# Kernel optimization log

Measured on AMD Instinct MI355X. Metric: run time of the kernel, lower is better.

Reference implementation:

```python
import jax, jax.numpy as jnp
import numpy as np

B, C, D, H, W = 2, 128, 16, 16, 16
DSIM = PSIM = GDIM = 64
N_ROUNDS = 3  # pool_strides = [1, 1, 1]


def build_neighbors(D, H, W):
    """Cross-graph neighbors: for node (i,j,k), all nodes sharing an axis line,
    self kept exactly once (dedup). Returns sorted [N, D+H+W-2] int indices."""
    N = D * H * W
    i, j, k = np.unravel_index(np.arange(N), (D, H, W))
    ax0 = np.arange(D)[None, :] * (H * W) + (j * W + k)[:, None]          # [N, D] (contains self)
    ax1 = (i * H * W)[:, None] + np.arange(H)[None, :] * W + k[:, None]   # [N, H]
    ax2 = (i * H * W + j * W)[:, None] + np.arange(W)[None, :]            # [N, W]
    self_idx = np.arange(N)
    ax1 = ax1[ax1 != self_idx[:, None]].reshape(N, H - 1)
    ax2 = ax2[ax2 != self_idx[:, None]].reshape(N, W - 1)
    return np.sort(np.concatenate([ax0, ax1, ax2], axis=1), axis=1)       # [N, D+H+W-2]


def l2norm(x, axis):
    return x / (1e-6 + jnp.linalg.norm(x, axis=axis, keepdims=True))


def setup_inputs() -> dict:
    key = jax.random.key(0)
    ks = jax.random.split(key, 13)
    s = 0.05
    return {
        "x": jax.random.normal(ks[0], (B, C, D, H, W), jnp.float32),
        "G_w": jax.random.normal(ks[1], (GDIM, C), jnp.float32) * s,
        "G_b": jax.random.normal(ks[2], (GDIM,), jnp.float32) * s,
        "theta_w": jax.random.normal(ks[3], (DSIM, C), jnp.float32) * s,
        "theta_b": jax.random.normal(ks[4], (DSIM,), jnp.float32) * s,
        "phi_w": jax.random.normal(ks[5], (DSIM, C), jnp.float32) * s,
        "phi_b": jax.random.normal(ks[6], (DSIM,), jnp.float32) * s,
        "r_w": jax.random.normal(ks[7], (C, GDIM), jnp.float32) * s,
        "r_b": jax.random.normal(ks[8], (C,), jnp.float32) * s,
        "geo_theta_w": jax.random.normal(ks[9], (PSIM, 3), jnp.float32) * s,
        "geo_theta_b": jax.random.normal(ks[10], (PSIM,), jnp.float32) * s,
        "geo_phi_w": jax.random.normal(ks[11], (PSIM, 3), jnp.float32) * s,
        "geo_phi_b": jax.random.normal(ks[12], (PSIM,), jnp.float32) * s,
    }


def reference(x, G_w, G_b, theta_w, theta_b, phi_w, phi_b, r_w, r_b,
              geo_theta_w, geo_theta_b, geo_phi_w, geo_phi_b):
    Bx, Cx, Dx, Hx, Wx = x.shape
    N = Dx * Hx * Wx
    nbr = jnp.asarray(build_neighbors(Dx, Hx, Wx))                         # [N, E]
    # geo positional features: normalized grid coords in [-0.5, 0.5], batch-identical
    coords = jnp.stack(jnp.meshgrid(jnp.arange(Dx), jnp.arange(Hx), jnp.arange(Wx),
                                    indexing='ij'), axis=-1).reshape(N, 3).astype(x.dtype)
    p = coords / (jnp.asarray([Dx, Hx, Wx], x.dtype) - 1.0) - 0.5          # [N, 3]
    p_theta = p @ geo_theta_w.T + geo_theta_b                              # [N, PSIM]
    p_phi = p @ geo_phi_w.T + geo_phi_b                                    # [N, PSIM]
    f_p = jnp.einsum('np,nep->ne', p_theta, p_phi[nbr])                    # [N, E]
    f_p = l2norm(f_p, axis=0)                                              # do_norm: l2 over node dim
    f_p = jax.nn.relu(f_p)[None]                                           # [1, N, E]

    h = x.reshape(Bx, Cx, N).transpose(0, 2, 1)                            # [B, N, C]
    for _ in range(N_ROUNDS):
        x_theta = h @ theta_w.T + theta_b                                  # [B, N, DSIM]
        x_phi_e = (h @ phi_w.T + phi_b)[:, nbr]                            # [B, N, E, DSIM]
        f = jnp.einsum('bnd,bned->bne', x_theta, x_phi_e)                  # [B, N, E]
        f = l2norm(f, axis=1)                                              # do_norm over node dim
        attn = jax.nn.softmax(f + f_p, axis=-1)                            # merge 'softmax'
        x_g_e = (h @ G_w.T + G_b)[:, nbr]                                  # [B, N, E, GDIM]
        y = jnp.einsum('bne,bneg->bng', attn, x_g_e)                       # [B, N, GDIM]
        h = h + (y @ r_w.T + r_b)                                          # residual (group_norm=False)
    return h.transpose(0, 2, 1).reshape(Bx, Cx, Dx, Hx, Wx)
```

## Files before the change

### kernel.cpp

```cpp
#include <hip/hip_runtime.h>
#include <math.h>

#define BB 2
#define CC 128
#define NN 4096
#define EE 46
#define FS 48
#define DS 64
#define CPAD 16
#define NSH 16

__global__ __launch_bounds__(256) void k_setup(
    const float* __restrict__ x,
    const float* __restrict__ gt_w, const float* __restrict__ gt_b,
    const float* __restrict__ gp_w, const float* __restrict__ gp_b,
    int* __restrict__ nbr, float* __restrict__ p_theta, float* __restrict__ p_phi,
    float* __restrict__ colnorm_p, float* __restrict__ colnorm_f,
    float* __restrict__ h)
{
    __shared__ float xs[32 * 65];
    const int t = threadIdx.x, bid = blockIdx.x;
    const int gtid = bid * 256 + t;

    if (gtid < EE * NSH * CPAD) colnorm_p[gtid] = 0.f;
    if (gtid < 3 * BB * EE * NSH * CPAD) colnorm_f[gtid] = 0.f;

    if (gtid < NN) {
        int n = gtid;
        int i = n >> 8, j = (n >> 4) & 15, k = n & 15;
        int ia = 0, ib = 0, ic = 0;
        for (int e = 0; e < EE; ++e) {
            int va = (ia < 16) ? ia * 256 + j * 16 + k : 0x7fffffff;
            int jb = ib + (ib >= j ? 1 : 0);
            int vb = (ib < 15) ? i * 256 + jb * 16 + k : 0x7fffffff;
            int kc = ic + (ic >= k ? 1 : 0);
            int vc = (ic < 15) ? i * 256 + j * 16 + kc : 0x7fffffff;
            int v;
            if (va < vb && va < vc)      { v = va; ++ia; }
            else if (vb < vc)            { v = vb; ++ib; }
            else                         { v = vc; ++ic; }
            nbr[n * EE + e] = v;
        }
    }
    for (int idx = gtid; idx < NN * DS; idx += 512 * 256) {
        int n = idx >> 6, s = idx & 63;
        int i = n >> 8, j = (n >> 4) & 15, k = n & 15;
        float p0 = i * (1.f / 15.f) - 0.5f;
        float p1 = j * (1.f / 15.f) - 0.5f;
        float p2 = k * (1.f / 15.f) - 0.5f;
        p_theta[idx] = p0 * gt_w[s * 3] + p1 * gt_w[s * 3 + 1] + p2 * gt_w[s * 3 + 2] + gt_b[s];
        p_phi[idx]   = p0 * gp_w[s * 3] + p1 * gp_w[s * 3 + 1] + p2 * gp_w[s * 3 + 2] + gp_b[s];
    }
    {
        int n0 = (bid & 63) * 64, c0 = ((bid >> 6) & 3) * 32, b = bid >> 8;
        for (int q = t; q < 2048; q += 256) {
            int cl = q >> 6, nl = q & 63;
            xs[cl * 65 + nl] = x[(size_t)(b * CC + c0 + cl) * NN + n0 + nl];
        }
        __syncthreads();
        for (int q = t; q < 2048; q += 256) {
            int nl = q >> 5, cl = q & 31;
            h[(size_t)(b * NN + n0 + nl) * CC + c0 + cl] = xs[cl * 65 + nl];
        }
    }
}

__global__ __launch_bounds__(256) void k_proj(
    const float* __restrict__ h,
    const float* __restrict__ th_w, const float* __restrict__ th_b,
    const float* __restrict__ ph_w, const float* __restrict__ ph_b,
    const float* __restrict__ G_w,  const float* __restrict__ G_b,
    float* __restrict__ T, float* __restrict__ P, float* __restrict__ Gx)
{
    __shared__ __align__(16) float smf[12288];
    const int t = threadIdx.x;
    const int row0 = (blockIdx.x & 255) * 32;
    const int cgp = blockIdx.x >> 8;
    const float* w    = cgp == 0 ? th_w : cgp == 1 ? ph_w : G_w;
    const float* bias = cgp == 0 ? th_b : cgp == 1 ? ph_b : G_b;
    float* o          = cgp == 0 ? T    : cgp == 1 ? P    : Gx;
    float4* hs4 = (float4*)smf;
    float4* ws4 = (float4*)smf + 1024;
    const float4* h4 = (const float4*)h;
    const float4* w4 = (const float4*)w;
    for (int q = t; q < 1024; q += 256) {
        int row = q >> 5, kc = q & 31;
        hs4[row * 32 + (kc ^ row)] = h4[(size_t)(row0 + row) * 32 + kc];
    }
    for (int q = t; q < 2048; q += 256) {
        int row = q >> 5, kc = q & 31;
        ws4[row * 32 + (kc ^ (row & 31))] = w4[q];
    }
    __syncthreads();
    const int rt = t >> 4, m = t & 15;
    float acc[2][4] = {{0, 0, 0, 0}, {0, 0, 0, 0}};
    for (int kc = 0; kc < 32; ++kc) {
        float4 a0 = hs4[(2 * rt) * 32 + (kc ^ (2 * rt))];
        float4 a1 = hs4[(2 * rt + 1) * 32 + (kc ^ (2 * rt + 1))];
        float4 wv[4];
#pragma unroll
        for (int i = 0; i < 4; ++i) {
            int c = m + 16 * i;
            wv[i] = ws4[c * 32 + (kc ^ (c & 31))];
        }
#pragma unroll
        for (int i = 0; i < 4; ++i) {
            acc[0][i] += a0.x * wv[i].x + a0.y * wv[i].y
                       + a0.z * wv[i].z + a0.w * wv[i].w;
            acc[1][i] += a1.x * wv[i].x + a1.y * wv[i].y
                       + a1.z * wv[i].z + a1.w * wv[i].w;
        }
    }
#pragma unroll
    for (int i = 0; i < 4; ++i) {
        float bv = bias[m + 16 * i];
#pragma unroll
        for (int rr = 0; rr < 2; ++rr)
            o[(size_t)(row0 + 2 * rt + rr) * DS + m + 16 * i] = acc[rr][i] + bv;
    }
}

__device__ __forceinline__ int axis_node(int axis, int line, int s) {
    if (axis == 0) return s * 256 + line;
    if (axis == 1) return (line >> 4) * 256 + s * 16 + (line & 15);
    return line * 16 + s;
}

__global__ __launch_bounds__(256) void k_fax(
    const float* __restrict__ T, const float* __restrict__ P,
    float* __restrict__ fax, float* __restrict__ colnorm)
{
    __shared__ __align__(16) float4 Ts4[272];
    __shared__ __align__(16) float4 Ps4[272];
    __shared__ float sq[64];

    const int t = threadIdx.x;
    const int line = blockIdx.x, axis = blockIdx.y, b = blockIdx.z;
    {
        int s = t >> 4, kc = t & 15;
        int nrow = axis_node(axis, line, s);
        Ts4[s * 17 + kc] = ((const float4*)T)[((size_t)b * NN + nrow) * 16 + kc];
        Ps4[s * 17 + kc] = ((const float4*)P)[((size_t)b * NN + nrow) * 16 + kc];
    }
    if (t < 64) sq[t] = 0.f;
    __syncthreads();

    const int node = t >> 4, slot = t & 15;
    const int n = axis_node(axis, line, node);
    const int m = axis_node(axis, line, slot);
    const int jj = (n >> 4) & 15, kk = n & 15;
    bool valid = !((axis == 1 && slot == jj) || (axis == 2 && slot == kk));

    float dot = 0.f;
#pragma unroll
    for (int kc = 0; kc < 16; ++kc) {
        float4 a = Ts4[node * 17 + kc];
        float4 p = Ps4[slot * 17 + kc];
        dot += a.x * p.x + a.y * p.y + a.z * p.z + a.w * p.w;
    }

    if (valid) {
        fax[((size_t)b * NN + n) * FS + axis * 16 + slot] = dot;
        const int jk = n & 255, base = n & ~255;
        int d = m - jk;
        int cD = d <= 0 ? 0 : min(16, (d + 255) >> 8);
        int hd = m - base - kk;
        int cHr = hd <= 0 ? 0 : min(16, (hd + 15) >> 4);
        int cH = cHr - (jj < cHr ? 1 : 0);
        int wd = m - (n - kk);
        int cWr = wd <= 0 ? 0 : min(16, wd);
        int cW = cWr - (kk < cWr ? 1 : 0);
        int e = cD + cH + cW;
        atomicAdd(&sq[e], dot * dot);
    }
    __syncthreads();
    if (t < EE)
        atomicAdd(colnorm + ((size_t)(b * EE + t) * NSH + (line & (NSH - 1))) * CPAD,
                  sq[t]);
}

__global__ __launch_bounds__(256) void k_agg(
    const int* __restrict__ nbr,
    const float* __restrict__ f, const float* __restrict__ f_p,
    const float* __restrict__ colnorm_p, const float* __restrict__ colnorm_f,
    const float* __restrict__ Gx, float* __restrict__ y)
{
    __shared__ __align__(16) float Gl[16 * 64];
    __shared__ float wmat[256];
    __shared__ float nf[64], np[64];

    const int t = threadIdx.x;
    const int line = blockIdx.x, axis = blockIdx.y, b = blockIdx.z;

    if (t < EE) {
        float sf = 0.f, sp = 0.f;
#pragma unroll
        for (int s = 0; s < NSH; ++s) {
            sf += colnorm_f[((size_t)(b * EE + t) * NSH + s) * CPAD];
            sp += colnorm_p[((size_t)t * NSH + s) * CPAD];
        }
        nf[t] = 1.f / (1e-6f + sqrtf(sf));
        np[t] = 1.f / (1e-6f + sqrtf(sp));
    }
    wmat[t] = 0.f;
    {
        int s = t >> 4, c4 = t & 15;
        int nrow = axis_node(axis, line, s);
        ((float4*)Gl)[s * 16 + c4] =
            ((const float4*)Gx)[((size_t)b * NN + nrow) * 16 + c4];
    }
    __syncthreads();

    const int wv = t >> 6, l = t & 63;
    for (int ii = 0; ii < 4; ++ii) {
        int sn = wv * 4 + ii;
        int n = axis_node(axis, line, sn);
        float fvv = -INFINITY; int ax = 0, slot = 0;
        if (l < EE) {
            int m = nbr[n * EE + l];
            int x = m ^ n;
            if (x == 0)       { ax = 0; slot = n >> 8; }
            else if (x < 16)  { ax = 2; slot = m & 15; }
            else if (x < 256) { ax = 1; slot = (m >> 4) & 15; }
            else              { ax = 0; slot = m >> 8; }
            int col = ax * 16 + slot;
            float fpv = f_p[(size_t)n * FS + col] * np[l];
            fpv = fpv > 0.f ? fpv : 0.f;
            fvv = f[(size_t)(b * NN + n) * FS + col] * nf[l] + fpv;
        }
        float mx = fvv;
        for (int o = 32; o; o >>= 1) mx = fmaxf(mx, __shfl_down(mx, o));
        mx = __shfl(mx, 0);
        float ex = (l < EE) ? expf(fvv - mx) : 0.f;
        float sm = ex;
        for (int o = 32; o; o >>= 1) sm += __shfl_down(sm, o);
        sm = __shfl(sm, 0);
        if (l < EE && ax == axis) wmat[sn * 16 + slot] = ex / sm;
    }
    __syncthreads();

    float acc[4] = {0.f, 0.f, 0.f, 0.f};
    for (int s = 0; s < 16; ++s) {
        float gv = Gl[s * 64 + l];
        acc[0] += wmat[(wv * 4 + 0) * 16 + s] * gv;
        acc[1] += wmat[(wv * 4 + 1) * 16 + s] * gv;
        acc[2] += wmat[(wv * 4 + 2) * 16 + s] * gv;
        acc[3] += wmat[(wv * 4 + 3) * 16 + s] * gv;
    }
    float* ya = y + ((size_t)axis * BB + b) * NN * DS;
#pragma unroll
    for (int kk = 0; kk < 4; ++kk) {
        int n = axis_node(axis, line, wv * 4 + kk);
        ya[(size_t)n * DS + l] = acc[kk];
    }
}

template <int LAST>
__global__ __launch_bounds__(256) void k_epi(
    const float* __restrict__ y, const float* __restrict__ r_w,
    const float* __restrict__ r_b,
    float* __restrict__ h, float* __restrict__ out)
{
    __shared__ __align__(16) float smf[6528];
    float4* ys4  = (float4*)smf;
    float4* rws4 = (float4*)smf + 544;
    float*  dls  = smf;

    const int t = threadIdx.x;
    const int rt0 = blockIdx.x * 32;
    const int c0 = blockIdx.y * 64;
    const float4* y4  = (const float4*)y;
    const float4* rw4 = (const float4*)r_w;
    for (int q = t; q < 512; q += 256) {
        int row = q >> 4, kc = q & 15;
        float4 a = y4[(size_t)(rt0 + row) * 16 + kc];
        float4 bb = y4[((size_t)BB * NN + rt0 + row) * 16 + kc];
        float4 c = y4[((size_t)2 * BB * NN + rt0 + row) * 16 + kc];
        float4 s;
        s.x = a.x + bb.x + c.x; s.y = a.y + bb.y + c.y;
        s.z = a.z + bb.z + c.z; s.w = a.w + bb.w + c.w;
        ys4[row * 17 + kc] = s;
    }
    for (int q = t; q < 1024; q += 256) {
        int row = q >> 4, kc = q & 15;
        rws4[row * 17 + kc] = rw4[(size_t)(c0 + row) * 16 + kc];
    }
    __syncthreads();

    const int rt = t >> 4, m = t & 15;
    float acc[2][4] = {{0, 0, 0, 0}, {0, 0, 0, 0}};
    for (int kc = 0; kc < 16; ++kc) {
        float4 a0 = ys4[(2 * rt) * 17 + kc];
        float4 a1 = ys4[(2 * rt + 1) * 17 + kc];
        float4 wv[4];
#pragma unroll
        for (int i = 0; i < 4; ++i)
            wv[i] = rws4[(m + 16 * i) * 17 + kc];
#pragma unroll
        for (int i = 0; i < 4; ++i) {
            acc[0][i] += a0.x * wv[i].x + a0.y * wv[i].y
                       + a0.z * wv[i].z + a0.w * wv[i].w;
            acc[1][i] += a1.x * wv[i].x + a1.y * wv[i].y
                       + a1.z * wv[i].z + a1.w * wv[i].w;
        }
    }

    if (!LAST) {
#pragma unroll
        for (int rr = 0; rr < 2; ++rr) {
            size_t r = (size_t)rt0 + 2 * rt + rr;
#pragma unroll
            for (int i = 0; i < 4; ++i) {
                int c = c0 + m + 16 * i;
                h[r * CC + c] += acc[rr][i] + r_b[c];
            }
        }
    } else {
        float res[2][4];
#pragma unroll
        for (int rr = 0; rr < 2; ++rr) {
            size_t r = (size_t)rt0 + 2 * rt + rr;
#pragma unroll
            for (int i = 0; i < 4; ++i) {
                int c = c0 + m + 16 * i;
                res[rr][i] = h[r * CC + c] + acc[rr][i] + r_b[c];
            }
        }
        __syncthreads();
#pragma unroll
        for (int rr = 0; rr < 2; ++rr)
#pragma unroll
            for (int i = 0; i < 4; ++i)
                dls[(2 * rt + rr) * 68 + m + 16 * i] = res[rr][i];
        __syncthreads();
        const int b = rt0 >> 12, n0g = rt0 & (NN - 1);
        for (int q = t; q < 2048; q += 256) {
            int cl = q >> 5, nl = q & 31;
            out[(size_t)(b * CC + c0 + cl) * NN + n0g + nl] = dls[nl * 68 + cl];
        }
    }
}

extern "C" void kernel_launch(void* const* d_in, const int* in_sizes, int n_in,
                              void* d_out, int out_size, void* d_ws, size_t ws_size,
                              hipStream_t stream) {
    const float* x    = (const float*)d_in[0];
    const float* G_w  = (const float*)d_in[1];
    const float* G_b  = (const float*)d_in[2];
    const float* th_w = (const float*)d_in[3];
    const float* th_b = (const float*)d_in[4];
    const float* ph_w = (const float*)d_in[5];
    const float* ph_b = (const float*)d_in[6];
    const float* r_w  = (const float*)d_in[7];
    const float* r_b  = (const float*)d_in[8];
    const float* gt_w = (const float*)d_in[9];
    const float* gt_b = (const float*)d_in[10];
    const float* gp_w = (const float*)d_in[11];
    const float* gp_b = (const float*)d_in[12];
    float* out = (float*)d_out;

    char* ws = (char*)d_ws;
    size_t off = 0;
    auto alloc = [&](size_t bytes) {
        char* p = ws + off;
        off = (off + bytes + 255) & ~size_t(255);
        return p;
    };
    int*   nbr       = (int*)  alloc((size_t)NN * EE * sizeof(int));
    float* p_theta   = (float*)alloc((size_t)NN * DS * sizeof(float));
    float* p_phi     = (float*)alloc((size_t)NN * DS * sizeof(float));
    float* f_p       = (float*)alloc((size_t)NN * FS * sizeof(float));
    float* colnorm_p = (float*)alloc((size_t)EE * NSH * CPAD * sizeof(float));
    float* colnorm_f = (float*)alloc((size_t)3 * BB * EE * NSH * CPAD * sizeof(float));
    float* h         = (float*)alloc((size_t)BB * NN * CC * sizeof(float));
    float* T         = (float*)alloc((size_t)BB * NN * DS * sizeof(float));
    float* P         = (float*)alloc((size_t)BB * NN * DS * sizeof(float));
    float* Gx        = (float*)alloc((size_t)BB * NN * DS * sizeof(float));
    float* f         = (float*)alloc((size_t)BB * NN * FS * sizeof(float));
    float* y         = (float*)alloc((size_t)3 * BB * NN * DS * sizeof(float));
    (void)ws_size; (void)in_sizes; (void)n_in; (void)out_size;

    k_setup<<<512, 256, 0, stream>>>(x, gt_w, gt_b, gp_w, gp_b, nbr,
                                     p_theta, p_phi, colnorm_p, colnorm_f, h);
    k_fax<<<dim3(256, 3, 1), 256, 0, stream>>>(p_theta, p_phi, f_p, colnorm_p);
    for (int r = 0; r < 3; ++r) {
        float* cn = colnorm_f + (size_t)r * BB * EE * NSH * CPAD;
        k_proj<<<768, 256, 0, stream>>>(h, th_w, th_b, ph_w, ph_b, G_w, G_b,
                                        T, P, Gx);
        k_fax<<<dim3(256, 3, BB), 256, 0, stream>>>(T, P, f, cn);
        k_agg<<<dim3(256, 3, BB), 256, 0, stream>>>(nbr, f, f_p, colnorm_p, cn,
                                                    Gx, y);
        if (r < 2)
            k_epi<0><<<dim3(256, 2), 256, 0, stream>>>(y, r_w, r_b, h, out);
        else
            k_epi<1><<<dim3(256, 2), 256, 0, stream>>>(y, r_w, r_b, h, out);
    }
}
```

Before: 168.6 us.

## Fuse residual projection into aggregation with atomics and compute neighbor ranks on the fly

Moves the r_w output projection and residual add into k_agg, where each per-axis block multiplies its partial y by r_w and atomically adds into h. This removes the y buffer round trip and the separate epilogue kernel each round. The neighbor table is no longer built; each lane computes its sorted edge rank analytically and permutes values through LDS. A final transpose kernel writes the output. In exchange, every block stages the full 128x64 r_w tile in LDS, the three axes contend on atomics into h, and float atomics make summation order nondeterministic.

New measurement: 293.2 us. +73.9%, slower.

```diff
diff --git a/kernel.cpp b/kernel.cpp
--- a/kernel.cpp
+++ b/kernel.cpp
@@ -14,7 +14,7 @@
     const float* __restrict__ x,
     const float* __restrict__ gt_w, const float* __restrict__ gt_b,
     const float* __restrict__ gp_w, const float* __restrict__ gp_b,
-    int* __restrict__ nbr, float* __restrict__ p_theta, float* __restrict__ p_phi,
+    float* __restrict__ p_theta, float* __restrict__ p_phi,
     float* __restrict__ colnorm_p, float* __restrict__ colnorm_f,
     float* __restrict__ h)
 {
@@ -25,23 +25,6 @@
     if (gtid < EE * NSH * CPAD) colnorm_p[gtid] = 0.f;
     if (gtid < 3 * BB * EE * NSH * CPAD) colnorm_f[gtid] = 0.f;
 
-    if (gtid < NN) {
-        int n = gtid;
-        int i = n >> 8, j = (n >> 4) & 15, k = n & 15;
-        int ia = 0, ib = 0, ic = 0;
-        for (int e = 0; e < EE; ++e) {
-            int va = (ia < 16) ? ia * 256 + j * 16 + k : 0x7fffffff;
-            int jb = ib + (ib >= j ? 1 : 0);
-            int vb = (ib < 15) ? i * 256 + jb * 16 + k : 0x7fffffff;
-            int kc = ic + (ic >= k ? 1 : 0);
-            int vc = (ic < 15) ? i * 256 + j * 16 + kc : 0x7fffffff;
-            int v;
-            if (va < vb && va < vc)      { v = va; ++ia; }
-            else if (vb < vc)            { v = vb; ++ib; }
-            else                         { v = vc; ++ic; }
-            nbr[n * EE + e] = v;
-        }
-    }
     for (int idx = gtid; idx < NN * DS; idx += 512 * 256) {
         int n = idx >> 6, s = idx & 63;
         int i = n >> 8, j = (n >> 4) & 15, k = n & 15;
@@ -180,18 +163,28 @@
 }
 
 __global__ __launch_bounds__(256) void k_agg(
-    const int* __restrict__ nbr,
+    const int* __restrict__ nbr2_unused,
     const float* __restrict__ f, const float* __restrict__ f_p,
     const float* __restrict__ colnorm_p, const float* __restrict__ colnorm_f,
-    const float* __restrict__ Gx, float* __restrict__ y)
+    const float* __restrict__ Gx,
+    const float* __restrict__ r_w, const float* __restrict__ r_b,
+    float* __restrict__ h)
 {
-    __shared__ __align__(16) float Gl[16 * 64];
-    __shared__ float wmat[256];
-    __shared__ float nf[64], np[64];
+    __shared__ __align__(16) float smf[10688];
+    float4* rws4 = (float4*)smf;
+    float*  ys   = smf + 8192;
+    float*  Gl   = smf + 9280;
+    float*  wmat = smf + 10304;
+    float*  nf   = smf + 10560;
+    float*  np   = smf + 10624;
 
     const int t = threadIdx.x;
     const int line = blockIdx.x, axis = blockIdx.y, b = blockIdx.z;
 
+    for (int i2 = t; i2 < 2048; i2 += 256) {
+        int c = i2 >> 4, g4 = i2 & 15;
+        rws4[c * 16 + ((g4 + c) & 15)] = ((const float4*)r_w)[i2];
+    }
     if (t < EE) {
         float sf = 0.f, sp = 0.f;
 #pragma unroll
@@ -217,16 +210,55 @@
         int n = axis_node(axis, line, sn);
         float fvv = -INFINITY; int ax = 0, slot = 0;
         if (l < EE) {
-            int m = nbr[n * EE + l];
-            int x = m ^ n;
-            if (x == 0)       { ax = 0; slot = n >> 8; }
-            else if (x < 16)  { ax = 2; slot = m & 15; }
-            else if (x < 256) { ax = 1; slot = (m >> 4) & 15; }
-            else              { ax = 0; slot = m >> 8; }
-            int col = ax * 16 + slot;
-            float fpv = f_p[(size_t)n * FS + col] * np[l];
-            fpv = fpv > 0.f ? fpv : 0.f;
-            fvv = f[(size_t)(b * NN + n) * FS + col] * nf[l] + fpv;
+            fvv = 0.f;
+        }
+        int cand_ax = 0, cand_slot = 0;
+        if (l < 16)      { cand_ax = 0; cand_slot = l; }
+        else if (l < 31) { int s2 = l - 16; cand_ax = 1; cand_slot = s2 + (s2 >= ((n >> 4) & 15) ? 1 : 0); }
+        else if (l < EE) { int s2 = l - 31; cand_ax = 2; cand_slot = s2 + (s2 >= (n & 15) ? 1 : 0); }
+        int m = axis_node(cand_ax, (cand_ax == 0) ? (n & 255)
+                   : (cand_ax == 1) ? (((n >> 8) << 4) | (n & 15))
+                   : (n >> 4), cand_slot);
+        int e_rank = 0;
+        if (l < EE) {
+            const int jj2 = (n >> 4) & 15, kk2 = n & 15;
+            const int jk = n & 255, base = n & ~255;
+            int d = m - jk;
+            int cD = d <= 0 ? 0 : min(16, (d + 255) >> 8);
+            int hd = m - base - kk2;
+            int cHr = hd <= 0 ? 0 : min(16, (hd + 15) >> 4);
+            int cH = cHr - (jj2 < cHr ? 1 : 0);
+            int wd = m - (n - kk2);
+            int cWr = wd <= 0 ? 0 : min(16, wd);
+            int cW = cWr - (kk2 < cWr ? 1 : 0);
+            e_rank = cD + cH + cW;
+        }
+        float fval = 0.f, fpval = 0.f;
+        if (l < EE) {
+            int col = cand_ax * 16 + cand_slot;
+            fval  = f[(size_t)(b * NN + n) * FS + col];
+            fpval = f_p[(size_t)n * FS + col];
+        }
+        float* perm = ys;
+        float* pv = perm + wv * 68;
+        if (l < EE) pv[e_rank] = fval;
+        __builtin_amdgcn_wave_barrier();
+        float f_sorted = (l < EE) ? pv[l] : 0.f;
+        __builtin_amdgcn_wave_barrier();
+        if (l < EE) pv[e_rank] = fpval;
+        __builtin_amdgcn_wave_barrier();
+        float fp_sorted = (l < EE) ? pv[l] : 0.f;
+        __builtin_amdgcn_wave_barrier();
+        if (l < EE) pv[e_rank] = (float)(cand_ax * 16 + cand_slot);
+        __builtin_amdgcn_wave_barrier();
+        int col_sorted = (l < EE) ? (int)pv[l] : 0;
+        __builtin_amdgcn_wave_barrier();
+
+        if (l < EE) {
+            float fpv2 = fp_sorted * np[l];
+            fpv2 = fpv2 > 0.f ? fpv2 : 0.f;
+            fvv = f_sorted * nf[l] + fpv2;
+            ax = col_sorted >> 4; slot = col_sorted & 15;
         }
         float mx = fvv;
         for (int o = 32; o; o >>= 1) mx = fmaxf(mx, __shfl_down(mx, o));
@@ -236,108 +268,65 @@
         for (int o = 32; o; o >>= 1) sm += __shfl_down(sm, o);
         sm = __shfl(sm, 0);
         if (l < EE && ax == axis) wmat[sn * 16 + slot] = ex / sm;
-    }
-    __syncthreads();
-
-    float acc[4] = {0.f, 0.f, 0.f, 0.f};
-    for (int s = 0; s < 16; ++s) {
-        float gv = Gl[s * 64 + l];
-        acc[0] += wmat[(wv * 4 + 0) * 16 + s] * gv;
-        acc[1] += wmat[(wv * 4 + 1) * 16 + s] * gv;
-        acc[2] += wmat[(wv * 4 + 2) * 16 + s] * gv;
-        acc[3] += wmat[(wv * 4 + 3) * 16 + s] * gv;
-    }
-    float* ya = y + ((size_t)axis * BB + b) * NN * DS;
-#pragma unroll
-    for (int kk = 0; kk < 4; ++kk) {
-        int n = axis_node(axis, line, wv * 4 + kk);
-        ya[(size_t)n * DS + l] = acc[kk];
-    }
-}
-
-template <int LAST>
-__global__ __launch_bounds__(256) void k_epi(
-    const float* __restrict__ y, const float* __restrict__ r_w,
-    const float* __restrict__ r_b,
-    float* __restrict__ h, float* __restrict__ out)
-{
-    __shared__ __align__(16) float smf[6528];
-    float4* ys4  = (float4*)smf;
-    float4* rws4 = (float4*)smf + 544;
-    float*  dls  = smf;
-
+        __builtin_amdgcn_wave_barrier();
+    }
+    __syncthreads();
+
+    {
+        float acc[4] = {0.f, 0.f, 0.f, 0.f};
+        for (int s = 0; s < 16; ++s) {
+            float gv = Gl[s * 64 + l];
+            acc[0] += wmat[(wv * 4 + 0) * 16 + s] * gv;
+            acc[1] += wmat[(wv * 4 + 1) * 16 + s] * gv;
+            acc[2] += wmat[(wv * 4 + 2) * 16 + s] * gv;
+            acc[3] += wmat[(wv * 4 + 3) * 16 + s] * gv;
+        }
+#pragma unroll
+        for (int kk = 0; kk < 4; ++kk)
+            ys[(wv * 4 + kk) * 68 + l] = acc[kk];
+    }
+    __syncthreads();
+
+    const int r0 = (t >> 5) * 2, cl = t & 31;
+    float4* ys4 = (float4*)ys;
+    float acc2[2][4] = {{0, 0, 0, 0}, {0, 0, 0, 0}};
+    for (int g4 = 0; g4 < 16; ++g4) {
+        float4 ya = ys4[r0 * 17 + g4];
+        float4 yb = ys4[(r0 + 1) * 17 + g4];
+#pragma unroll
+        for (int cc = 0; cc < 4; ++cc) {
+            int c = cl + 32 * cc;
+            float4 w = rws4[c * 16 + ((g4 + c) & 15)];
+            acc2[0][cc] += ya.x * w.x + ya.y * w.y + ya.z * w.z + ya.w * w.w;
+            acc2[1][cc] += yb.x * w.x + yb.y * w.y + yb.z * w.z + yb.w * w.w;
+        }
+    }
+#pragma unroll
+    for (int rr = 0; rr < 2; ++rr) {
+        int n = axis_node(axis, line, r0 + rr);
+        size_t bn = (size_t)b * NN + n;
+#pragma unroll
+        for (int cc = 0; cc < 4; ++cc) {
+            int c = cl + 32 * cc;
+            float add = acc2[rr][cc] + (axis == 0 ? r_b[c] : 0.f);
+            atomicAdd(&h[bn * CC + c], add);
+        }
+    }
+}
+
+__global__ __launch_bounds__(256) void k_out(const float* __restrict__ h,
+                                             float* __restrict__ out) {
+    __shared__ float hs_[64][33];
     const int t = threadIdx.x;
-    const int rt0 = blockIdx.x * 32;
-    const int c0 = blockIdx.y * 64;
-    const float4* y4  = (const float4*)y;
-    const float4* rw4 = (const float4*)r_w;
-    for (int q = t; q < 512; q += 256) {
-        int row = q >> 4, kc = q & 15;
-        float4 a = y4[(size_t)(rt0 + row) * 16 + kc];
-        float4 bb = y4[((size_t)BB * NN + rt0 + row) * 16 + kc];
-        float4 c = y4[((size_t)2 * BB * NN + rt0 + row) * 16 + kc];
-        float4 s;
-        s.x = a.x + bb.x + c.x; s.y = a.y + bb.y + c.y;
-        s.z = a.z + bb.z + c.z; s.w = a.w + bb.w + c.w;
-        ys4[row * 17 + kc] = s;
-    }
-    for (int q = t; q < 1024; q += 256) {
-        int row = q >> 4, kc = q & 15;
-        rws4[row * 17 + kc] = rw4[(size_t)(c0 + row) * 16 + kc];
-    }
-    __syncthreads();
-
-    const int rt = t >> 4, m = t & 15;
-    float acc[2][4] = {{0, 0, 0, 0}, {0, 0, 0, 0}};
-    for (int kc = 0; kc < 16; ++kc) {
-        float4 a0 = ys4[(2 * rt) * 17 + kc];
-        float4 a1 = ys4[(2 * rt + 1) * 17 + kc];
-        float4 wv[4];
-#pragma unroll
-        for (int i = 0; i < 4; ++i)
-            wv[i] = rws4[(m + 16 * i) * 17 + kc];
-#pragma unroll
-        for (int i = 0; i < 4; ++i) {
-            acc[0][i] += a0.x * wv[i].x + a0.y * wv[i].y
-                       + a0.z * wv[i].z + a0.w * wv[i].w;
-            acc[1][i] += a1.x * wv[i].x + a1.y * wv[i].y
-                       + a1.z * wv[i].z + a1.w * wv[i].w;
-        }
-    }
-
-    if (!LAST) {
-#pragma unroll
-        for (int rr = 0; rr < 2; ++rr) {
-            size_t r = (size_t)rt0 + 2 * rt + rr;
-#pragma unroll
-            for (int i = 0; i < 4; ++i) {
-                int c = c0 + m + 16 * i;
-                h[r * CC + c] += acc[rr][i] + r_b[c];
-            }
-        }
-    } else {
-        float res[2][4];
-#pragma unroll
-        for (int rr = 0; rr < 2; ++rr) {
-            size_t r = (size_t)rt0 + 2 * rt + rr;
-#pragma unroll
-            for (int i = 0; i < 4; ++i) {
-                int c = c0 + m + 16 * i;
-                res[rr][i] = h[r * CC + c] + acc[rr][i] + r_b[c];
-            }
-        }
-        __syncthreads();
-#pragma unroll
-        for (int rr = 0; rr < 2; ++rr)
-#pragma unroll
-            for (int i = 0; i < 4; ++i)
-                dls[(2 * rt + rr) * 68 + m + 16 * i] = res[rr][i];
-        __syncthreads();
-        const int b = rt0 >> 12, n0g = rt0 & (NN - 1);
-        for (int q = t; q < 2048; q += 256) {
-            int cl = q >> 5, nl = q & 31;
-            out[(size_t)(b * CC + c0 + cl) * NN + n0g + nl] = dls[nl * 68 + cl];
-        }
+    const int n0 = blockIdx.x * 64, c0 = blockIdx.y * 32, b = blockIdx.z;
+    for (int q = t; q < 2048; q += 256) {
+        int nl = q >> 5, cl = q & 31;
+        hs_[nl][cl] = h[(size_t)(b * NN + n0 + nl) * CC + c0 + cl];
+    }
+    __syncthreads();
+    for (int q = t; q < 2048; q += 256) {
+        int cl = q >> 6, nl = q & 63;
+        out[(size_t)(b * CC + c0 + cl) * NN + n0 + nl] = hs_[nl][cl];
     }
 }
 
@@ -366,7 +355,6 @@
         off = (off + bytes + 255) & ~size_t(255);
         return p;
     };
-    int*   nbr       = (int*)  alloc((size_t)NN * EE * sizeof(int));
     float* p_theta   = (float*)alloc((size_t)NN * DS * sizeof(float));
     float* p_phi     = (float*)alloc((size_t)NN * DS * sizeof(float));
     float* f_p       = (float*)alloc((size_t)NN * FS * sizeof(float));
@@ -377,10 +365,9 @@
     float* P         = (float*)alloc((size_t)BB * NN * DS * sizeof(float));
     float* Gx        = (float*)alloc((size_t)BB * NN * DS * sizeof(float));
     float* f         = (float*)alloc((size_t)BB * NN * FS * sizeof(float));
-    float* y         = (float*)alloc((size_t)3 * BB * NN * DS * sizeof(float));
     (void)ws_size; (void)in_sizes; (void)n_in; (void)out_size;
 
-    k_setup<<<512, 256, 0, stream>>>(x, gt_w, gt_b, gp_w, gp_b, nbr,
+    k_setup<<<512, 256, 0, stream>>>(x, gt_w, gt_b, gp_w, gp_b,
                                      p_theta, p_phi, colnorm_p, colnorm_f, h);
     k_fax<<<dim3(256, 3, 1), 256, 0, stream>>>(p_theta, p_phi, f_p, colnorm_p);
     for (int r = 0; r < 3; ++r) {
@@ -388,11 +375,9 @@
         k_proj<<<768, 256, 0, stream>>>(h, th_w, th_b, ph_w, ph_b, G_w, G_b,
                                         T, P, Gx);
         k_fax<<<dim3(256, 3, BB), 256, 0, stream>>>(T, P, f, cn);
-        k_agg<<<dim3(256, 3, BB), 256, 0, stream>>>(nbr, f, f_p, colnorm_p, cn,
-                                                    Gx, y);
-        if (r < 2)
-            k_epi<0><<<dim3(256, 2), 256, 0, stream>>>(y, r_w, r_b, h, out);
-        else
-            k_epi<1><<<dim3(256, 2), 256, 0, stream>>>(y, r_w, r_b, h, out);
-    }
-}
+        k_agg<<<dim3(256, 3, BB), 256, 0, stream>>>(nullptr, f, f_p,
+                                                    colnorm_p, cn, Gx,
+                                                    r_w, r_b, h);
+    }
+    k_out<<<dim3(64, 4, 2), 256, 0, stream>>>(h, out);
+}
```
